# Performance work log

Hardware: AMD Instinct MI355X
Metric: run time of the kernel (lower is better)

Reference implementation:

```python
import jax, jax.numpy as jnp
import numpy as np

N_NODES = 65536
N_EDGES = 524288
FEAT_DIM = 512
EMBED_DIM = 512


def setup_inputs() -> dict:
    key = jax.random.key(0)
    k1, k2, k3, k4, k5 = jax.random.split(key, 5)
    x = jax.random.normal(k1, (N_NODES, FEAT_DIM), dtype=jnp.float32)
    # xavier_uniform for (embed_dim, feat_dim)
    limit = float(np.sqrt(6.0 / (EMBED_DIM + FEAT_DIM)))
    weight = jax.random.uniform(k2, (EMBED_DIM, FEAT_DIM), dtype=jnp.float32,
                                minval=-limit, maxval=limit)
    row = jax.random.randint(k3, (N_EDGES,), 0, N_NODES, dtype=jnp.int64)
    col = jax.random.randint(k4, (N_EDGES,), 0, N_NODES, dtype=jnp.int64)
    vals = jax.random.uniform(k5, (N_EDGES,), dtype=jnp.float32)
    return {"x": x, "weight": weight, "row": row, "col": col, "vals": vals}


def reference(x, weight, row, col, vals):
    # Fused GEMM + SpMM: out = adj @ (x @ weight.T)
    h = jnp.einsum('nf,ef->ne', x, weight)            # [N, embed_dim] dense GEMM
    msgs = vals[:, None] * h[col]                     # [E, embed_dim] gather + scale
    out = jax.ops.segment_sum(msgs, row, num_segments=N_NODES)  # SpMM scatter-add
    return out
```

## Files before the change

### kernel.cpp

```cpp
#include <hip/hip_runtime.h>
#include <stdint.h>


#define N_NODES 65536
#define N_EDGES 524288
#define FEAT    512
#define EMB     512
#define CAP     64
#define CNTS    16

typedef short  short8  __attribute__((ext_vector_type(8)));
typedef float  floatx4 __attribute__((ext_vector_type(4)));
typedef unsigned int uintx2 __attribute__((ext_vector_type(2)));

__device__ __forceinline__ unsigned short f2bf(float f) {
    unsigned int u = __float_as_uint(f);
    u += 0x7FFFu + ((u >> 16) & 1u);
    return (unsigned short)(u >> 16);
}
__device__ __forceinline__ float bf2f_lo(unsigned int u){ return __uint_as_float(u << 16); }
__device__ __forceinline__ float bf2f_hi(unsigned int u){ return __uint_as_float(u & 0xffff0000u); }

typedef __attribute__((address_space(1))) const void* gas_vp;
typedef __attribute__((address_space(3))) void*       las_vp;
#define GLDS16(g, l) __builtin_amdgcn_global_load_lds((gas_vp)(const void*)(g), (las_vp)(void*)(l), 16, 0, 0)

__global__ __launch_bounds__(256)
void conv_bf16(const float* __restrict__ in, unsigned short* __restrict__ out)
{
    size_t i = ((size_t)blockIdx.x * 256 + threadIdx.x) * 8;
    floatx4 a = __builtin_nontemporal_load((const floatx4*)&in[i]);
    floatx4 b = __builtin_nontemporal_load((const floatx4*)&in[i + 4]);
    ushort4 lo, hi;
    lo.x = f2bf(a.x); lo.y = f2bf(a.y); lo.z = f2bf(a.z); lo.w = f2bf(a.w);
    hi.x = f2bf(b.x); hi.y = f2bf(b.y); hi.z = f2bf(b.z); hi.w = f2bf(b.w);
    *(ushort4*)&out[i]     = lo;
    *(ushort4*)&out[i + 4] = hi;
}

__global__ __launch_bounds__(512, 4)
void gemm_fused(const float* __restrict__ x, const unsigned short* __restrict__ wb,
                unsigned short* __restrict__ h)
{
    __shared__ unsigned short As[64 * 64];
    __shared__ unsigned short Bs[512 * 64];

    const int t    = threadIdx.x;
    const int lane = t & 63;
    const int wave = t >> 6;
    const int l15  = lane & 15;
    const int lq   = lane >> 4;

    const int m0 = blockIdx.x * 64;

    const int r8 = t >> 3;
    const int c8 = t & 7;

    floatx4 acc[4][4];
    #pragma unroll
    for (int i = 0; i < 4; i++)
        #pragma unroll
        for (int j = 0; j < 4; j++) acc[i][j] = (floatx4){0.f, 0.f, 0.f, 0.f};

    float4 xa, xb_;
    {
        const float* px = &x[(size_t)(m0 + r8) * FEAT + c8 * 8];
        xa  = *(const float4*)px;
        xb_ = *(const float4*)(px + 4);
    }

    for (int kb = 0; kb < FEAT; kb += 64) {
        #pragma unroll
        for (int p = 0; p < 8; p++) {
            int row = p * 64 + r8;
            int lc  = c8 ^ (r8 & 7);
            GLDS16(&wb[row * FEAT + kb + lc * 8], &Bs[row * 64 + c8 * 8]);
        }
        {
            short8 v;
            v[0] = (short)f2bf(xa.x);  v[1] = (short)f2bf(xa.y);
            v[2] = (short)f2bf(xa.z);  v[3] = (short)f2bf(xa.w);
            v[4] = (short)f2bf(xb_.x); v[5] = (short)f2bf(xb_.y);
            v[6] = (short)f2bf(xb_.z); v[7] = (short)f2bf(xb_.w);
            *(short8*)&As[r8 * 64 + (c8 ^ (r8 & 7)) * 8] = v;
        }
        __syncthreads();

        if (kb + 64 < FEAT) {
            const float* px = &x[(size_t)(m0 + r8) * FEAT + (kb + 64) + c8 * 8];
            xa  = *(const float4*)px;
            xb_ = *(const float4*)(px + 4);
        }

        #pragma unroll
        for (int kk = 0; kk < 2; kk++) {
            short8 af[4], bfr[4];
            #pragma unroll
            for (int mt = 0; mt < 4; mt++) {
                int r  = mt * 16 + l15;
                int pc = (kk * 4 + lq) ^ (r & 7);
                af[mt] = *(const short8*)&As[r * 64 + pc * 8];
            }
            #pragma unroll
            for (int nt = 0; nt < 4; nt++) {
                int r  = wave * 64 + nt * 16 + l15;
                int pc = (kk * 4 + lq) ^ (r & 7);
                bfr[nt] = *(const short8*)&Bs[r * 64 + pc * 8];
            }
            #pragma unroll
            for (int mt = 0; mt < 4; mt++)
                #pragma unroll
                for (int nt = 0; nt < 4; nt++)
                    acc[mt][nt] = __builtin_amdgcn_mfma_f32_16x16x32_bf16(
                        af[mt], bfr[nt], acc[mt][nt], 0, 0, 0);
        }
        __syncthreads();
    }

    #pragma unroll
    for (int mt = 0; mt < 4; mt++)
        #pragma unroll
        for (int nt = 0; nt < 4; nt++)
            #pragma unroll
            for (int r = 0; r < 4; r++) {
                int row = m0 + mt * 16 + lq * 4 + r;
                int col = wave * 64 + nt * 16 + l15;
                h[(size_t)row * EMB + col] = f2bf(acc[mt][nt][r]);
            }
}

#define BM 128
#define BN 64
#define LDA 72

__global__ __launch_bounds__(256)
void gemm_f32(const float* __restrict__ x, const float* __restrict__ w,
              unsigned short* __restrict__ h)
{
    __shared__ unsigned short As[BM][LDA];
    __shared__ unsigned short Bs[BN][LDA];

    const int t = threadIdx.x, lane = t & 63, wave = t >> 6;
    const int wm = wave >> 1, wn = wave & 1;
    const int l15 = lane & 15, lq = lane >> 4;
    const int xcd = blockIdx.x & 7;
    const int loc = blockIdx.x >> 3;
    const int m0 = (xcd * 64 + (loc >> 3)) * BM;
    const int n0 = (loc & 7) * BN;

    floatx4 acc[4][2];
    #pragma unroll
    for (int i = 0; i < 4; i++)
        #pragma unroll
        for (int j = 0; j < 2; j++) acc[i][j] = (floatx4){0.f, 0.f, 0.f, 0.f};

    for (int kb = 0; kb < FEAT; kb += 64) {
        #pragma unroll
        for (int p = 0; p < 8; p++) {
            int idx = p * 256 + t, row = idx >> 4, cv = (idx & 15) << 2;
            float4 v = *(const float4*)&x[(m0 + row) * FEAT + kb + cv];
            ushort4 b4 = {f2bf(v.x), f2bf(v.y), f2bf(v.z), f2bf(v.w)};
            *(ushort4*)&As[row][cv] = b4;
        }
        #pragma unroll
        for (int p = 0; p < 4; p++) {
            int idx = p * 256 + t, row = idx >> 4, cv = (idx & 15) << 2;
            float4 v = *(const float4*)&w[(n0 + row) * FEAT + kb + cv];
            ushort4 b4 = {f2bf(v.x), f2bf(v.y), f2bf(v.z), f2bf(v.w)};
            *(ushort4*)&Bs[row][cv] = b4;
        }
        __syncthreads();
        #pragma unroll
        for (int kk = 0; kk < 2; kk++) {
            short8 af[4], bf[2];
            #pragma unroll
            for (int mt = 0; mt < 4; mt++)
                af[mt] = *(const short8*)&As[wm * 64 + mt * 16 + l15][kk * 32 + lq * 8];
            #pragma unroll
            for (int nt = 0; nt < 2; nt++)
                bf[nt] = *(const short8*)&Bs[wn * 32 + nt * 16 + l15][kk * 32 + lq * 8];
            #pragma unroll
            for (int mt = 0; mt < 4; mt++)
                #pragma unroll
                for (int nt = 0; nt < 2; nt++)
                    acc[mt][nt] = __builtin_amdgcn_mfma_f32_16x16x32_bf16(
                        af[mt], bf[nt], acc[mt][nt], 0, 0, 0);
        }
        __syncthreads();
    }
    #pragma unroll
    for (int mt = 0; mt < 4; mt++)
        #pragma unroll
        for (int nt = 0; nt < 2; nt++)
            #pragma unroll
            for (int r = 0; r < 4; r++) {
                int row = m0 + wm * 64 + mt * 16 + lq * 4 + r;
                int col = n0 + wn * 32 + nt * 16 + l15;
                h[row * EMB + col] = f2bf(acc[mt][nt][r]);
            }
}

__global__ __launch_bounds__(256)
void fill_edges(const int* __restrict__ row, const int* __restrict__ col,
                const float* __restrict__ vals, int* __restrict__ cnt,
                uintx2* __restrict__ ebuf)
{
    int e = blockIdx.x * 256 + threadIdx.x;
    int   r = __builtin_nontemporal_load(&row[e]);
    int   c = __builtin_nontemporal_load(&col[e]);
    float v = __builtin_nontemporal_load(&vals[e]);
    int slot = atomicAdd(&cnt[(size_t)r * CNTS], 1);
    if (slot < CAP) {
        uintx2 ev; ev.x = (unsigned)c; ev.y = __float_as_uint(v);
        ebuf[r * CAP + slot] = ev;
    }
}

__global__ __launch_bounds__(256)
void rowsum(const unsigned short* __restrict__ h, const int* __restrict__ cnt,
            const uintx2* __restrict__ ebuf, float* __restrict__ out, int rbase)
{
    const int r    = rbase + blockIdx.x * 4 + (threadIdx.x >> 6);
    const int lane = threadIdx.x & 63;
    int deg = cnt[(size_t)r * CNTS];
    if (deg > CAP) deg = CAP;
    const int base = r * CAP;

    int   c_l = 0;
    float v_l = 0.f;
    if (lane < deg) {
        uintx2 ev = ebuf[base + lane];
        c_l = (int)ev.x;
        v_l = __uint_as_float(ev.y);
    }

    float acc[8] = {0.f,0.f,0.f,0.f,0.f,0.f,0.f,0.f};
    for (int i0 = 0; i0 < deg; i0 += 8) {
        uint4 hv[8]; float vv[8];
        int nn = deg - i0; if (nn > 8) nn = 8;
        #pragma unroll
        for (int j = 0; j < 8; j++) {
            if (j < nn) {
                int c = __shfl(c_l, i0 + j, 64);
                vv[j] = __shfl(v_l, i0 + j, 64);
                hv[j] = *(const uint4*)&h[(size_t)c * EMB + lane * 8];
            }
        }
        #pragma unroll
        for (int j = 0; j < 8; j++) {
            if (j < nn) {
                float v = vv[j];
                acc[0] += v * bf2f_lo(hv[j].x); acc[1] += v * bf2f_hi(hv[j].x);
                acc[2] += v * bf2f_lo(hv[j].y); acc[3] += v * bf2f_hi(hv[j].y);
                acc[4] += v * bf2f_lo(hv[j].z); acc[5] += v * bf2f_hi(hv[j].z);
                acc[6] += v * bf2f_lo(hv[j].w); acc[7] += v * bf2f_hi(hv[j].w);
            }
        }
    }
    floatx4* o = (floatx4*)&out[(size_t)r * EMB + lane * 8];
    floatx4 o0; o0.x = acc[0]; o0.y = acc[1]; o0.z = acc[2]; o0.w = acc[3];
    floatx4 o1; o1.x = acc[4]; o1.y = acc[5]; o1.z = acc[6]; o1.w = acc[7];
    __builtin_nontemporal_store(o0, o);
    __builtin_nontemporal_store(o1, o + 1);
}

__global__ __launch_bounds__(128)
void scatter_atomic(const int* __restrict__ row, const int* __restrict__ col,
                    const float* __restrict__ vals, const unsigned short* __restrict__ h,
                    float* __restrict__ out)
{
    int e = blockIdx.x;
    int r = row[e], c = col[e];
    float v = vals[e];
    int f = threadIdx.x * 4;
    uint2 hv = *(const uint2*)&h[c * EMB + f];
    float* o = &out[r * EMB + f];
    atomicAdd(o + 0, v * bf2f_lo(hv.x));
    atomicAdd(o + 1, v * bf2f_hi(hv.x));
    atomicAdd(o + 2, v * bf2f_lo(hv.y));
    atomicAdd(o + 3, v * bf2f_hi(hv.y));
}

extern "C" void kernel_launch(void* const* d_in, const int* in_sizes, int n_in,
                              void* d_out, int out_size, void* d_ws, size_t ws_size,
                              hipStream_t stream) {
    const float* x    = (const float*)d_in[0];
    const float* w    = (const float*)d_in[1];
    const int*   row  = (const int*)d_in[2];
    const int*   col  = (const int*)d_in[3];
    const float* vals = (const float*)d_in[4];
    float* out = (float*)d_out;
    char* ws = (char*)d_ws;

    const size_t SZ_WB  = (size_t)EMB * FEAT * 2;
    const size_t SZ_H   = (size_t)N_NODES * EMB * 2;
    const size_t SZ_CNT = (size_t)N_NODES * CNTS * 4;
    const size_t SZ_E   = (size_t)N_NODES * CAP * 8;
    const size_t NEED_FAST = SZ_WB + SZ_H + SZ_CNT + SZ_E;
    const size_t NEED_BIN  = SZ_H + SZ_CNT + SZ_E;

    if (ws_size >= NEED_FAST) {
        unsigned short* wb = (unsigned short*)ws;
        unsigned short* h  = (unsigned short*)(ws + SZ_WB);
        int*    cnt  = (int*)(ws + SZ_WB + SZ_H);
        uintx2* ebuf = (uintx2*)(ws + SZ_WB + SZ_H + SZ_CNT);

        conv_bf16<<<dim3((EMB * FEAT) / (256 * 8)), dim3(256), 0, stream>>>(w, wb);
        gemm_fused<<<dim3(N_NODES / 64), dim3(512), 0, stream>>>(x, wb, h);
        (void)hipMemsetAsync(cnt, 0, SZ_CNT, stream);
        fill_edges<<<dim3(N_EDGES / 256), dim3(256), 0, stream>>>(row, col, vals, cnt, ebuf);
        rowsum<<<dim3(N_NODES / 8), dim3(256), 0, stream>>>(h, cnt, ebuf, out, 0);
        rowsum<<<dim3(N_NODES / 8), dim3(256), 0, stream>>>(h, cnt, ebuf, out, N_NODES / 2);
    } else if (ws_size >= NEED_BIN) {
        unsigned short* h = (unsigned short*)ws;
        int*    cnt  = (int*)(ws + SZ_H);
        uintx2* ebuf = (uintx2*)(ws + SZ_H + SZ_CNT);

        gemm_f32<<<dim3(4096), dim3(256), 0, stream>>>(x, w, h);
        (void)hipMemsetAsync(cnt, 0, SZ_CNT, stream);
        fill_edges<<<dim3(N_EDGES / 256), dim3(256), 0, stream>>>(row, col, vals, cnt, ebuf);
        rowsum<<<dim3(N_NODES / 8), dim3(256), 0, stream>>>(h, cnt, ebuf, out, 0);
        rowsum<<<dim3(N_NODES / 8), dim3(256), 0, stream>>>(h, cnt, ebuf, out, N_NODES / 2);
    } else {
        unsigned short* h = (unsigned short*)ws;
        gemm_f32<<<dim3(4096), dim3(256), 0, stream>>>(x, w, h);
        (void)hipMemsetAsync(out, 0, (size_t)out_size * sizeof(float), stream);
        scatter_atomic<<<dim3(N_EDGES), dim3(128), 0, stream>>>(row, col, vals, h, out);
    }
}
```

Before: 388.8 us.

## Fuse edge binning into GEMM kernel, zero counters in prep, merge rowsum launches

Interleaves edge-binning blocks (odd block indices) with GEMM tile blocks in one launch, so the atomic binning runs alongside the MFMA GEMM instead of as a separate kernel. Counter zeroing moves into the weight-conversion prep kernel, replacing the memset. The padded counter stride (16 ints per node) is dropped for a dense array, and the two half-range rowsum launches become one. This removes launches and idle gaps between them, but dense counters may bring more atomic contention on shared cache lines, and binning blocks use the GEMM kernel's LDS footprint, which can limit occupancy.

Measured after the change: 410.7 us. 5.6% more time.

```diff
diff --git a/kernel.cpp b/kernel.cpp
--- a/kernel.cpp
+++ b/kernel.cpp
@@ -7,7 +7,6 @@
 #define FEAT    512
 #define EMB     512
 #define CAP     64
-#define CNTS    16
 
 typedef short  short8  __attribute__((ext_vector_type(8)));
 typedef float  floatx4 __attribute__((ext_vector_type(4)));
@@ -26,32 +25,53 @@
 #define GLDS16(g, l) __builtin_amdgcn_global_load_lds((gas_vp)(const void*)(g), (las_vp)(void*)(l), 16, 0, 0)
 
 __global__ __launch_bounds__(256)
-void conv_bf16(const float* __restrict__ in, unsigned short* __restrict__ out)
-{
-    size_t i = ((size_t)blockIdx.x * 256 + threadIdx.x) * 8;
-    floatx4 a = __builtin_nontemporal_load((const floatx4*)&in[i]);
-    floatx4 b = __builtin_nontemporal_load((const floatx4*)&in[i + 4]);
+void prep(const float* __restrict__ w, unsigned short* __restrict__ wb,
+          int* __restrict__ cnt)
+{
+    size_t i = (size_t)blockIdx.x * 256 + threadIdx.x;
+    size_t j = i * 8;
+    floatx4 a = *(const floatx4*)&w[j];
+    floatx4 b = *(const floatx4*)&w[j + 4];
     ushort4 lo, hi;
     lo.x = f2bf(a.x); lo.y = f2bf(a.y); lo.z = f2bf(a.z); lo.w = f2bf(a.w);
     hi.x = f2bf(b.x); hi.y = f2bf(b.y); hi.z = f2bf(b.z); hi.w = f2bf(b.w);
-    *(ushort4*)&out[i]     = lo;
-    *(ushort4*)&out[i + 4] = hi;
+    *(ushort4*)&wb[j]     = lo;
+    *(ushort4*)&wb[j + 4] = hi;
+    int2 z; z.x = 0; z.y = 0;
+    *(int2*)&cnt[i * 2] = z;
 }
 
 __global__ __launch_bounds__(512, 4)
-void gemm_fused(const float* __restrict__ x, const unsigned short* __restrict__ wb,
-                unsigned short* __restrict__ h)
+void gemm_fill(const float* __restrict__ x, const unsigned short* __restrict__ wb,
+               unsigned short* __restrict__ h,
+               const int* __restrict__ row, const int* __restrict__ col,
+               const float* __restrict__ vals,
+               int* __restrict__ cnt, uintx2* __restrict__ ebuf)
 {
     __shared__ unsigned short As[64 * 64];
     __shared__ unsigned short Bs[512 * 64];
 
+    if (blockIdx.x & 1) {
+        int e = (blockIdx.x >> 1) * 512 + threadIdx.x;
+        int   r = __builtin_nontemporal_load(&row[e]);
+        int   c = __builtin_nontemporal_load(&col[e]);
+        float v = __builtin_nontemporal_load(&vals[e]);
+        int slot = atomicAdd(&cnt[r], 1);
+        if (slot < CAP) {
+            uintx2 ev; ev.x = (unsigned)c; ev.y = __float_as_uint(v);
+            ebuf[r * CAP + slot] = ev;
+        }
+        return;
+    }
+
+    const int gid  = blockIdx.x >> 1;
     const int t    = threadIdx.x;
     const int lane = t & 63;
     const int wave = t >> 6;
     const int l15  = lane & 15;
     const int lq   = lane >> 4;
 
-    const int m0 = blockIdx.x * 64;
+    const int m0 = gid * 64;
 
     const int r8 = t >> 3;
     const int c8 = t & 7;
@@ -72,9 +92,9 @@
     for (int kb = 0; kb < FEAT; kb += 64) {
         #pragma unroll
         for (int p = 0; p < 8; p++) {
-            int row = p * 64 + r8;
-            int lc  = c8 ^ (r8 & 7);
-            GLDS16(&wb[row * FEAT + kb + lc * 8], &Bs[row * 64 + c8 * 8]);
+            int brow = p * 64 + r8;
+            int lc   = c8 ^ (r8 & 7);
+            GLDS16(&wb[brow * FEAT + kb + lc * 8], &Bs[brow * 64 + c8 * 8]);
         }
         {
             short8 v;
@@ -123,9 +143,9 @@
         for (int nt = 0; nt < 4; nt++)
             #pragma unroll
             for (int r = 0; r < 4; r++) {
-                int row = m0 + mt * 16 + lq * 4 + r;
-                int col = wave * 64 + nt * 16 + l15;
-                h[(size_t)row * EMB + col] = f2bf(acc[mt][nt][r]);
+                int orow = m0 + mt * 16 + lq * 4 + r;
+                int ocol = wave * 64 + nt * 16 + l15;
+                h[(size_t)orow * EMB + ocol] = f2bf(acc[mt][nt][r]);
             }
 }
 
@@ -137,8 +157,8 @@
 void gemm_f32(const float* __restrict__ x, const float* __restrict__ w,
               unsigned short* __restrict__ h)
 {
-    __shared__ unsigned short As[BM][LDA];
-    __shared__ unsigned short Bs[BN][LDA];
+    __shared__ unsigned short As2[BM][LDA];
+    __shared__ unsigned short Bs2[BN][LDA];
 
     const int t = threadIdx.x, lane = t & 63, wave = t >> 6;
     const int wm = wave >> 1, wn = wave & 1;
@@ -157,17 +177,17 @@
     for (int kb = 0; kb < FEAT; kb += 64) {
         #pragma unroll
         for (int p = 0; p < 8; p++) {
-            int idx = p * 256 + t, row = idx >> 4, cv = (idx & 15) << 2;
-            float4 v = *(const float4*)&x[(m0 + row) * FEAT + kb + cv];
+            int idx = p * 256 + t, r = idx >> 4, cv = (idx & 15) << 2;
+            float4 v = *(const float4*)&x[(m0 + r) * FEAT + kb + cv];
             ushort4 b4 = {f2bf(v.x), f2bf(v.y), f2bf(v.z), f2bf(v.w)};
-            *(ushort4*)&As[row][cv] = b4;
+            *(ushort4*)&As2[r][cv] = b4;
         }
         #pragma unroll
         for (int p = 0; p < 4; p++) {
-            int idx = p * 256 + t, row = idx >> 4, cv = (idx & 15) << 2;
-            float4 v = *(const float4*)&w[(n0 + row) * FEAT + kb + cv];
+            int idx = p * 256 + t, r = idx >> 4, cv = (idx & 15) << 2;
+            float4 v = *(const float4*)&w[(n0 + r) * FEAT + kb + cv];
             ushort4 b4 = {f2bf(v.x), f2bf(v.y), f2bf(v.z), f2bf(v.w)};
-            *(ushort4*)&Bs[row][cv] = b4;
+            *(ushort4*)&Bs2[r][cv] = b4;
         }
         __syncthreads();
         #pragma unroll
@@ -175,10 +195,10 @@
             short8 af[4], bf[2];
             #pragma unroll
             for (int mt = 0; mt < 4; mt++)
-                af[mt] = *(const short8*)&As[wm * 64 + mt * 16 + l15][kk * 32 + lq * 8];
+                af[mt] = *(const short8*)&As2[wm * 64 + mt * 16 + l15][kk * 32 + lq * 8];
             #pragma unroll
             for (int nt = 0; nt < 2; nt++)
-                bf[nt] = *(const short8*)&Bs[wn * 32 + nt * 16 + l15][kk * 32 + lq * 8];
+                bf[nt] = *(const short8*)&Bs2[wn * 32 + nt * 16 + l15][kk * 32 + lq * 8];
             #pragma unroll
             for (int mt = 0; mt < 4; mt++)
                 #pragma unroll
@@ -194,9 +214,9 @@
         for (int nt = 0; nt < 2; nt++)
             #pragma unroll
             for (int r = 0; r < 4; r++) {
-                int row = m0 + wm * 64 + mt * 16 + lq * 4 + r;
-                int col = n0 + wn * 32 + nt * 16 + l15;
-                h[row * EMB + col] = f2bf(acc[mt][nt][r]);
+                int orow = m0 + wm * 64 + mt * 16 + lq * 4 + r;
+                int ocol = n0 + wn * 32 + nt * 16 + l15;
+                h[orow * EMB + ocol] = f2bf(acc[mt][nt][r]);
             }
 }
 
@@ -209,7 +229,7 @@
     int   r = __builtin_nontemporal_load(&row[e]);
     int   c = __builtin_nontemporal_load(&col[e]);
     float v = __builtin_nontemporal_load(&vals[e]);
-    int slot = atomicAdd(&cnt[(size_t)r * CNTS], 1);
+    int slot = atomicAdd(&cnt[r], 1);
     if (slot < CAP) {
         uintx2 ev; ev.x = (unsigned)c; ev.y = __float_as_uint(v);
         ebuf[r * CAP + slot] = ev;
@@ -218,11 +238,11 @@
 
 __global__ __launch_bounds__(256)
 void rowsum(const unsigned short* __restrict__ h, const int* __restrict__ cnt,
-            const uintx2* __restrict__ ebuf, float* __restrict__ out, int rbase)
-{
-    const int r    = rbase + blockIdx.x * 4 + (threadIdx.x >> 6);
+            const uintx2* __restrict__ ebuf, float* __restrict__ out)
+{
+    const int r    = blockIdx.x * 4 + (threadIdx.x >> 6);
     const int lane = threadIdx.x & 63;
-    int deg = cnt[(size_t)r * CNTS];
+    int deg = cnt[r];
     if (deg > CAP) deg = CAP;
     const int base = r * CAP;
 
@@ -294,7 +314,7 @@
 
     const size_t SZ_WB  = (size_t)EMB * FEAT * 2;
     const size_t SZ_H   = (size_t)N_NODES * EMB * 2;
-    const size_t SZ_CNT = (size_t)N_NODES * CNTS * 4;
+    const size_t SZ_CNT = (size_t)N_NODES * 4;
     const size_t SZ_E   = (size_t)N_NODES * CAP * 8;
     const size_t NEED_FAST = SZ_WB + SZ_H + SZ_CNT + SZ_E;
     const size_t NEED_BIN  = SZ_H + SZ_CNT + SZ_E;
@@ -305,12 +325,9 @@
         int*    cnt  = (int*)(ws + SZ_WB + SZ_H);
         uintx2* ebuf = (uintx2*)(ws + SZ_WB + SZ_H + SZ_CNT);
 
-        conv_bf16<<<dim3((EMB * FEAT) / (256 * 8)), dim3(256), 0, stream>>>(w, wb);
-        gemm_fused<<<dim3(N_NODES / 64), dim3(512), 0, stream>>>(x, wb, h);
-        (void)hipMemsetAsync(cnt, 0, SZ_CNT, stream);
-        fill_edges<<<dim3(N_EDGES / 256), dim3(256), 0, stream>>>(row, col, vals, cnt, ebuf);
-        rowsum<<<dim3(N_NODES / 8), dim3(256), 0, stream>>>(h, cnt, ebuf, out, 0);
-        rowsum<<<dim3(N_NODES / 8), dim3(256), 0, stream>>>(h, cnt, ebuf, out, N_NODES / 2);
+        prep<<<dim3(128), dim3(256), 0, stream>>>(w, wb, cnt);
+        gemm_fill<<<dim3(2048), dim3(512), 0, stream>>>(x, wb, h, row, col, vals, cnt, ebuf);
+        rowsum<<<dim3(N_NODES / 4), dim3(256), 0, stream>>>(h, cnt, ebuf, out);
     } else if (ws_size >= NEED_BIN) {
         unsigned short* h = (unsigned short*)ws;
         int*    cnt  = (int*)(ws + SZ_H);
@@ -319,8 +336,7 @@
         gemm_f32<<<dim3(4096), dim3(256), 0, stream>>>(x, w, h);
         (void)hipMemsetAsync(cnt, 0, SZ_CNT, stream);
         fill_edges<<<dim3(N_EDGES / 256), dim3(256), 0, stream>>>(row, col, vals, cnt, ebuf);
-        rowsum<<<dim3(N_NODES / 8), dim3(256), 0, stream>>>(h, cnt, ebuf, out, 0);
-        rowsum<<<dim3(N_NODES / 8), dim3(256), 0, stream>>>(h, cnt, ebuf, out, N_NODES / 2);
+        rowsum<<<dim3(N_NODES / 4), dim3(256), 0, stream>>>(h, cnt, ebuf, out);
     } else {
         unsigned short* h = (unsigned short*)ws;
         gemm_f32<<<dim3(4096), dim3(256), 0, stream>>>(x, w, h);
```
